# Kernel optimization log

Hardware: AMD Instinct MI355X
Metric: run time of the kernel (lower is better)

Reference implementation:

```python
import jax, jax.numpy as jnp
import numpy as np

B, S, H = 2, 1024, 2048
HQ, HKV, D = 16, 4, 128
E, K, CAP = 32, 4, 512
IM, SIM = 512, 1024
EPS = 1e-6
THETA = 1.0e6
T = B * S


def setup_inputs() -> dict:
    key = jax.random.key(0)
    ks = jax.random.split(key, 16)
    r = lambda i, shape, s=0.02: jax.random.normal(ks[i], shape, dtype=jnp.float32) * s
    return {
        "hidden_states": jax.random.normal(ks[0], (T, H), dtype=jnp.float32),
        "positions": jnp.tile(jnp.arange(S, dtype=jnp.int32), B),
        "ln1_w": jnp.ones((H,), jnp.float32),
        "ln2_w": jnp.ones((H,), jnp.float32),
        "wq": r(1, (H, HQ * D)),
        "wk": r(2, (H, HKV * D)),
        "wv": r(3, (H, HKV * D)),
        "wo": r(4, (HQ * D, H)),
        "qn_w": jnp.ones((D,), jnp.float32),
        "kn_w": jnp.ones((D,), jnp.float32),
        "gate_w": r(5, (H, E), 0.05),
        "expert_bias": r(6, (E,), 0.1),
        "w_gate_e": r(7, (E, H, IM)),
        "w_up_e": r(8, (E, H, IM)),
        "w_down_e": r(9, (E, IM, H)),
        "ws_gate": r(10, (H, SIM)),
        "ws_up": r(11, (H, SIM)),
        "ws_down": r(12, (SIM, H)),
    }


def _rms(x, w):
    return x * jax.lax.rsqrt(jnp.mean(x * x, axis=-1, keepdims=True) + EPS) * w


def _forward(hidden_states, positions, ln1_w, ln2_w, wq, wk, wv, wo, qn_w, kn_w,
             gate_w, expert_bias, w_gate_e, w_up_e, w_down_e, ws_gate, ws_up, ws_down):
    # --- attention block ---
    resid = hidden_states
    h = _rms(hidden_states, ln1_w)
    q = (h @ wq).reshape(T, HQ, D)
    k = (h @ wk).reshape(T, HKV, D)
    v = (h @ wv).reshape(T, HKV, D)
    q = _rms(q, qn_w)  # per-head qk-norm
    k = _rms(k, kn_w)
    # neox-style RoPE over full head_dim
    inv = 1.0 / (THETA ** (jnp.arange(0, D, 2, dtype=jnp.float32) / D))
    fr = positions.astype(jnp.float32)[:, None] * inv  # [T, D/2]
    cos, sin = jnp.cos(fr)[:, None, :], jnp.sin(fr)[:, None, :]
    def rope(x):
        x1, x2 = jnp.split(x, 2, axis=-1)
        return jnp.concatenate([x1 * cos - x2 * sin, x2 * cos + x1 * sin], axis=-1)
    q, k = rope(q), rope(k)
    qb = q.reshape(B, S, HQ, D)
    kb = jnp.repeat(k.reshape(B, S, HKV, D), HQ // HKV, axis=2)  # GQA expand
    vb = jnp.repeat(v.reshape(B, S, HKV, D), HQ // HKV, axis=2)
    sc = jnp.einsum('bqhd,bkhd->bhqk', qb, kb) * (D ** -0.5)
    causal = jnp.tril(jnp.ones((S, S), dtype=bool))
    sc = jnp.where(causal, sc, jnp.float32(-1e30))
    p = jax.nn.softmax(sc, axis=-1)
    ao = jnp.einsum('bhqk,bkhd->bqhd', p, vb).reshape(T, HQ * D)
    h = ao @ wo + resid
    resid = h
    h = _rms(h, ln2_w)
    # --- shared experts (dense MLP) ---
    shared = (jax.nn.silu(h @ ws_gate) * (h @ ws_up)) @ ws_down
    # --- sigmoid router with correction bias (bias only for selection) ---
    scores = jax.nn.sigmoid(h @ gate_w)          # [T, E]
    _, idx = jax.lax.top_k(scores + expert_bias, K)
    w = jnp.take_along_axis(scores, idx, axis=-1)
    w = w / jnp.sum(w, axis=-1, keepdims=True)   # renormalize top-k probs
    # --- capacity-based dispatch / grouped GEMM / combine ---
    flat_e = idx.reshape(-1)                     # [T*K]
    flat_t = jnp.repeat(jnp.arange(T), K)
    flat_w = w.reshape(-1)
    order = jnp.argsort(flat_e)                  # stable sort by expert
    se, st, sw = flat_e[order], flat_t[order], flat_w[order]
    counts = jnp.bincount(flat_e, length=E)
    starts = jnp.concatenate([jnp.zeros((1,), counts.dtype), jnp.cumsum(counts)[:-1]])
    pos = jnp.arange(T * K) - starts[se]         # slot within expert
    valid = pos < CAP                            # capacity guard (never trips in practice)
    posc = jnp.minimum(pos, CAP - 1)
    xbuf = jnp.zeros((E, CAP, H), h.dtype).at[se, posc].add(
        jnp.where(valid[:, None], h[st], 0.0))   # [E, CAP, H]
    inter = jax.nn.silu(jnp.einsum('ech,ehi->eci', xbuf, w_gate_e)) \
            * jnp.einsum('ech,ehi->eci', xbuf, w_up_e)
    obuf = jnp.einsum('eci,eih->ech', inter, w_down_e)
    y = obuf[se, posc] * jnp.where(valid, sw, 0.0)[:, None]
    moe = jnp.zeros((T, H), h.dtype).at[st].add(y)
    return resid + moe + shared


def reference(hidden_states, positions, ln1_w, ln2_w, wq, wk, wv, wo, qn_w, kn_w,
              gate_w, expert_bias, w_gate_e, w_up_e, w_down_e, ws_gate, ws_up, ws_down):
    return _forward(hidden_states, positions, ln1_w, ln2_w, wq, wk, wv, wo, qn_w, kn_w,
                    gate_w, expert_bias, w_gate_e, w_up_e, w_down_e, ws_gate, ws_up, ws_down)
```

## Files before the change

kernel.cpp:

```cpp
#include <hip/hip_runtime.h>
#include <stdint.h>

typedef unsigned short u16;
typedef unsigned short bf16u;
typedef unsigned int u32;
typedef _Float16 f16;
typedef __attribute__((ext_vector_type(8))) short bf16x8;
typedef __attribute__((ext_vector_type(8))) _Float16 f16x8;
typedef __attribute__((ext_vector_type(4))) float f32x4;

#define T_N 2048
#define H_N 2048
#define S_N 1024
#define B_N 2
#define HQ_N 16
#define HKV_N 4
#define D_N 128
#define E_N 32
#define K_TOP 4
#define CAP_N 512
#define IM_N 512
#define SIM_N 1024
#define QD_N 2048
#define KD_N 512
#define QKV_N 3072
#define NFLAT (T_N*K_TOP)
#define RGRP 128
#define NGRP (NFLAT/RGRP)

#define SC_H1   1024.0f
#define SC_W    512.0f
#define SC_QK   2048.0f
#define SC_P    4096.0f
#define SC_V    2048.0f
#define OSC_QKV (1.0f/524288.0f)
#define OSC_OPJ (1.0f/1048576.0f)

__device__ __forceinline__ float bf2f(bf16u x){ return __uint_as_float(((u32)x)<<16); }
__device__ __forceinline__ bf16u f2bf(float f){
  u32 u = __float_as_uint(f);
  u32 r = (u + 0x7FFFu + ((u>>16)&1u)) >> 16;
  return (bf16u)r;
}
__device__ __forceinline__ u32 pkbf(float a, float b){
  u32 ua = __float_as_uint(a), ub = __float_as_uint(b);
  u32 ra = (ua + 0x7FFFu + ((ua>>16)&1u)) >> 16;
  u32 rb = (ub + 0x7FFFu + ((ub>>16)&1u)) & 0xFFFF0000u;
  return ra | rb;
}
__device__ __forceinline__ void split2h(float x, u16& h, u16& l){
  f16 hh = (f16)x;
  f16 ll = (f16)(x - (float)hh);
  h = __builtin_bit_cast(u16, hh);
  l = __builtin_bit_cast(u16, ll);
}
__device__ __forceinline__ f32x4 mfma16b(bf16x8 a, bf16x8 b, f32x4 c){
  return __builtin_amdgcn_mfma_f32_16x16x32_bf16(a,b,c,0,0,0);
}
__device__ __forceinline__ f32x4 mfma16h(f16x8 a, f16x8 b, f32x4 c){
  return __builtin_amdgcn_mfma_f32_16x16x32_f16(a,b,c,0,0,0);
}
__device__ __forceinline__ void gl_lds16(const void* g, void* l){
  __builtin_amdgcn_global_load_lds((const __attribute__((address_space(1))) u32*)g,
                                   (__attribute__((address_space(3))) u32*)l, 16, 0, 0);
}

__global__ __launch_bounds__(256) void transpose_f32(const float* __restrict__ in,
                                                     float* __restrict__ out, int R, int C){
  __shared__ float tile[32][33];
  int rb = blockIdx.x*32, cb = blockIdx.y*32;
  int tx = threadIdx.x, ty = threadIdx.y;
  #pragma unroll
  for (int kk=0;kk<4;kk++)
    tile[ty+kk*8][tx] = in[(size_t)(rb+ty+kk*8)*C + cb + tx];
  __syncthreads();
  #pragma unroll
  for (int kk=0;kk<4;kk++)
    out[(size_t)(cb+ty+kk*8)*R + rb + tx] = tile[tx][ty+kk*8];
}

__global__ __launch_bounds__(256) void transpose_cvt_g(const float* __restrict__ in,
                                                       bf16u* __restrict__ out, int R, int C){
  __shared__ float tile[64*64];
  size_t zo = (size_t)blockIdx.z * R * C;
  int rb = blockIdx.x*64, cb = blockIdx.y*64;
  int tid = threadIdx.x, wave = tid>>6, lane = tid&63;
  #pragma unroll
  for (int p=0;p<4;p++){
    int r = p*16 + wave*4 + (lane>>4);
    const float* src = in + zo + (size_t)(rb + r)*C + cb + (lane&15)*4;
    gl_lds16(src, &tile[(p*16 + wave*4)*64]);
  }
  __syncthreads();
  int c = tid>>2, rq = (tid&3)*16;
  u16 tmp[16];
  #pragma unroll
  for (int j=0;j<16;j++) tmp[j] = f2bf(tile[(rq+j)*64 + c]);
  uint4 w0, w1;
  w0.x=(u32)tmp[0]|((u32)tmp[1]<<16);  w0.y=(u32)tmp[2]|((u32)tmp[3]<<16);
  w0.z=(u32)tmp[4]|((u32)tmp[5]<<16);  w0.w=(u32)tmp[6]|((u32)tmp[7]<<16);
  w1.x=(u32)tmp[8]|((u32)tmp[9]<<16);  w1.y=(u32)tmp[10]|((u32)tmp[11]<<16);
  w1.z=(u32)tmp[12]|((u32)tmp[13]<<16); w1.w=(u32)tmp[14]|((u32)tmp[15]<<16);
  bf16u* dst = out + zo + (size_t)(cb+c)*R + rb + rq;
  *(uint4*)dst = w0;
  *(uint4*)(dst+8) = w1;
}

__global__ __launch_bounds__(256) void transpose_cvt_split16(const float* __restrict__ in,
                                                             u16* __restrict__ oh,
                                                             u16* __restrict__ ol,
                                                             int R, int C, float scale){
  __shared__ u16 th[32][33];
  __shared__ u16 tl[32][33];
  int rb = blockIdx.x*32, cb = blockIdx.y*32;
  int tx = threadIdx.x, ty = threadIdx.y;
  #pragma unroll
  for (int kk=0;kk<4;kk++){
    float x = in[(size_t)(rb+ty+kk*8)*C + cb + tx] * scale;
    u16 hh, ll; split2h(x, hh, ll);
    th[ty+kk*8][tx] = hh; tl[ty+kk*8][tx] = ll;
  }
  __syncthreads();
  #pragma unroll
  for (int kk=0;kk<4;kk++){
    size_t idx = (size_t)(cb+ty+kk*8)*R + rb + tx;
    oh[idx] = th[tx][ty+kk*8];
    ol[idx] = tl[tx][ty+kk*8];
  }
}

__global__ __launch_bounds__(256) void rmsnorm_bf16(const float* __restrict__ x,
                                                    const float* __restrict__ w,
                                                    bf16u* __restrict__ y){
  int row = blockIdx.x; int t = threadIdx.x;
  const float4* x4 = (const float4*)(x + (size_t)row*H_N);
  float4 a = x4[2*t], b = x4[2*t+1];
  float ss = a.x*a.x+a.y*a.y+a.z*a.z+a.w*a.w + b.x*b.x+b.y*b.y+b.z*b.z+b.w*b.w;
  #pragma unroll
  for (int m=32;m>=1;m>>=1) ss += __shfl_xor(ss,m,64);
  __shared__ float red[4];
  if ((t&63)==0) red[t>>6]=ss;
  __syncthreads();
  float scale = rsqrtf((red[0]+red[1]+red[2]+red[3])*(1.0f/H_N) + 1e-6f);
  const float4* w4 = (const float4*)w;
  float4 wa = w4[2*t], wb = w4[2*t+1];
  uint4 pk;
  pk.x = pkbf(a.x*scale*wa.x, a.y*scale*wa.y);
  pk.y = pkbf(a.z*scale*wa.z, a.w*scale*wa.w);
  pk.z = pkbf(b.x*scale*wb.x, b.y*scale*wb.y);
  pk.w = pkbf(b.z*scale*wb.z, b.w*scale*wb.w);
  ((uint4*)(y + (size_t)row*H_N))[t] = pk;
}

__global__ __launch_bounds__(256) void rmsnorm_f16split(const float* __restrict__ x,
                                                        const float* __restrict__ w,
                                                        u16* __restrict__ yh,
                                                        u16* __restrict__ yl){
  int row = blockIdx.x; int t = threadIdx.x;
  const float4* x4 = (const float4*)(x + (size_t)row*H_N);
  float4 a = x4[2*t], b = x4[2*t+1];
  float ss = a.x*a.x+a.y*a.y+a.z*a.z+a.w*a.w + b.x*b.x+b.y*b.y+b.z*b.z+b.w*b.w;
  #pragma unroll
  for (int m=32;m>=1;m>>=1) ss += __shfl_xor(ss,m,64);
  __shared__ float red[4];
  if ((t&63)==0) red[t>>6]=ss;
  __syncthreads();
  float scale = rsqrtf((red[0]+red[1]+red[2]+red[3])*(1.0f/H_N) + 1e-6f) * SC_H1;
  const float4* w4 = (const float4*)w;
  float4 wa = w4[2*t], wb = w4[2*t+1];
  float o[8] = {a.x*scale*wa.x, a.y*scale*wa.y, a.z*scale*wa.z, a.w*scale*wa.w,
                b.x*scale*wb.x, b.y*scale*wb.y, b.z*scale*wb.z, b.w*scale*wb.w};
  u16 hh[8], ll[8];
  #pragma unroll
  for (int j=0;j<8;j++) split2h(o[j], hh[j], ll[j]);
  uint4 pk, pl;
  pk.x = (u32)hh[0]|((u32)hh[1]<<16); pk.y = (u32)hh[2]|((u32)hh[3]<<16);
  pk.z = (u32)hh[4]|((u32)hh[5]<<16); pk.w = (u32)hh[6]|((u32)hh[7]<<16);
  pl.x = (u32)ll[0]|((u32)ll[1]<<16); pl.y = (u32)ll[2]|((u32)ll[3]<<16);
  pl.z = (u32)ll[4]|((u32)ll[5]<<16); pl.w = (u32)ll[6]|((u32)ll[7]<<16);
  ((uint4*)(yh + (size_t)row*H_N))[t] = pk;
  ((uint4*)(yl + (size_t)row*H_N))[t] = pl;
}

__global__ void qknorm_rope_split(const float* __restrict__ qkv,
                                  const float* __restrict__ qw, const float* __restrict__ kw,
                                  const int* __restrict__ positions,
                                  u16* __restrict__ qho, u16* __restrict__ qlo,
                                  u16* __restrict__ kho, u16* __restrict__ klo){
  int t = blockIdx.x; int hy = blockIdx.y; int l = threadIdx.x;
  const float* p; const float* w; u16 *oh, *ol; size_t obase;
  if (hy < HQ_N){
    p = qkv + (size_t)t*QKV_N + hy*D_N; w = qw;
    oh = qho; ol = qlo; obase = (size_t)t*QD_N + hy*D_N;
  } else {
    p = qkv + (size_t)t*QKV_N + QD_N + (hy-HQ_N)*D_N; w = kw;
    oh = kho; ol = klo; obase = (size_t)t*KD_N + (hy-HQ_N)*D_N;
  }
  float x0 = p[l], x1 = p[l+64];
  float ss = x0*x0 + x1*x1;
  #pragma unroll
  for (int m=32;m>=1;m>>=1) ss += __shfl_xor(ss,m,64);
  float scale = rsqrtf(ss*(1.0f/D_N)+1e-6f);
  x0 *= scale*w[l]; x1 *= scale*w[l+64];
  double freq = exp2(-(double)l * (19.931568569324174/64.0));
  double fr = (double)positions[t] * freq;
  double sd, cd; sincos(fr, &sd, &cd);
  float r0 = (float)((double)x0*cd - (double)x1*sd) * SC_QK;
  float r1 = (float)((double)x1*cd + (double)x0*sd) * SC_QK;
  u16 hh, ll;
  split2h(r0, hh, ll); oh[obase+l] = hh; ol[obase+l] = ll;
  split2h(r1, hh, ll); oh[obase+l+64] = hh; ol[obase+l+64] = ll;
}

__global__ __launch_bounds__(256) void transpose_v_split(const float* __restrict__ in,
                                                         u16* __restrict__ oh,
                                                         u16* __restrict__ ol){
  __shared__ u16 th[32][33];
  __shared__ u16 tl[32][33];
  int z = blockIdx.z; int b = z >> 2, kvh = z & 3;
  const float* ip = in + (size_t)b*S_N*QKV_N + QD_N + KD_N + kvh*D_N;
  size_t ob = (size_t)z*D_N*S_N;
  int sb = blockIdx.x*32, db = blockIdx.y*32;
  int tx=threadIdx.x, ty=threadIdx.y;
  #pragma unroll
  for (int kk=0;kk<4;kk++){
    float x = ip[(size_t)(sb+ty+kk*8)*QKV_N + db+tx] * SC_V;
    u16 hh, ll; split2h(x, hh, ll);
    th[ty+kk*8][tx] = hh; tl[ty+kk*8][tx] = ll;
  }
  __syncthreads();
  #pragma unroll
  for (int kk=0;kk<4;kk++){
    size_t idx = ob + (size_t)(db+ty+kk*8)*S_N + sb+tx;
    oh[idx] = th[tx][ty+kk*8];
    ol[idx] = tl[tx][ty+kk*8];
  }
}

template<int MODE, bool SPLIT>
__global__ __launch_bounds__(256) void gemm_bt(
    const u16* __restrict__ A, const u16* __restrict__ Al,
    const u16* __restrict__ B0g, const u16* __restrict__ B0lg,
    const u16* __restrict__ B1g,
    void* __restrict__ Cout, const float* __restrict__ resid, float oscale,
    int N, int Kd,
    const int* __restrict__ startsA, const int* __restrict__ countsA,
    const int* __restrict__ perm)
{
  constexpr bool DUAL = (MODE==2 || MODE==3);
  constexpr bool MOE  = (MODE==3 || MODE==4);
  __shared__ u16 As[2][128*32];
  __shared__ u16 Bs0[2][128*32];
  __shared__ u16 Asl[SPLIT?2:1][SPLIT?128*32:8];
  __shared__ u16 Bs0l[SPLIT?2:1][SPLIT?128*32:8];
  __shared__ u16 Bs1[DUAL?2:1][DUAL?128*32:8];

  int tid = threadIdx.x;
  int wave = tid>>6, lane = tid&63, l15 = lane&15, lg = lane>>4;
  int nBase = blockIdx.y*128;

  int mBase, rows, slotBase=0;
  const u16* Bp0 = B0g; const u16* Bp1 = B1g;
  if constexpr (MOE){
    int e = blockIdx.z;
    int cnt = countsA[e]; cnt = cnt < CAP_N ? cnt : CAP_N;
    mBase = blockIdx.x*128;
    rows = cnt - mBase;
    if (rows <= 0) return;
    if (rows > 128) rows = 128;
    slotBase = startsA[e] + mBase;
    Bp0 = B0g + (size_t)e*N*Kd;
    if constexpr (DUAL) Bp1 = B1g + (size_t)e*N*Kd;
  } else { mBase = blockIdx.x*128; rows = 128; }

  size_t aOff[2], bOff[2];
  #pragma unroll
  for (int i=0;i<2;i++){
    int le = (i*256 + tid)*8;
    int r = le >> 5;
    int c = le & 31;
    int rr = (r < rows) ? r : 0;
    size_t arow;
    if constexpr (MODE==3) arow = (size_t)perm[slotBase + rr];
    else if constexpr (MODE==4) arow = (size_t)(slotBase + rr);
    else arow = (size_t)(mBase + r);
    aOff[i] = arow*Kd + c;
    bOff[i] = (size_t)(nBase + r)*Kd + c;
  }

  auto STAGE = [&](int buf, int kt){
    size_t ko = (size_t)kt*32;
    #pragma unroll
    for (int i=0;i<2;i++){
      int lo = i*2048 + wave*512;
      gl_lds16(A + aOff[i] + ko, &As[buf][lo]);
      gl_lds16(Bp0 + bOff[i] + ko, &Bs0[buf][lo]);
      if constexpr (SPLIT){
        gl_lds16(Al + aOff[i] + ko, &Asl[buf][lo]);
        gl_lds16(B0lg + bOff[i] + ko, &Bs0l[buf][lo]);
      }
      if constexpr (DUAL){
        gl_lds16(Bp1 + bOff[i] + ko, &Bs1[buf][lo]);
      }
    }
  };

  f32x4 zero4 = {0.f,0.f,0.f,0.f};
  f32x4 acc0[4][4];
  f32x4 acc1[DUAL?4:1][DUAL?4:1];
  #pragma unroll
  for (int mi=0;mi<4;mi++)
    #pragma unroll
    for (int ni=0;ni<4;ni++){
      acc0[mi][ni] = zero4;
      if constexpr (DUAL) acc1[mi][ni] = zero4;
    }

  int wm = wave>>1, wn = wave&1;
  int nK = Kd >> 5;
  STAGE(0, 0);
  __syncthreads();
  for (int kt=0; kt<nK; kt++){
    int cur = kt&1;
    if (kt+1 < nK) STAGE(cur^1, kt+1);
    if constexpr (SPLIT){
      f16x8 af[4], afl[4];
      #pragma unroll
      for (int mi=0;mi<4;mi++){
        af[mi]  = *(const f16x8*)&As [cur][(wm*64 + mi*16 + l15)*32 + lg*8];
        afl[mi] = *(const f16x8*)&Asl[cur][(wm*64 + mi*16 + l15)*32 + lg*8];
      }
      #pragma unroll
      for (int ni=0;ni<4;ni++){
        f16x8 b0  = *(const f16x8*)&Bs0 [cur][(wn*64 + ni*16 + l15)*32 + lg*8];
        f16x8 b0l = *(const f16x8*)&Bs0l[cur][(wn*64 + ni*16 + l15)*32 + lg*8];
        #pragma unroll
        for (int mi=0;mi<4;mi++){
          acc0[mi][ni] = mfma16h(af[mi], b0, acc0[mi][ni]);
          acc0[mi][ni] = mfma16h(af[mi], b0l, acc0[mi][ni]);
          acc0[mi][ni] = mfma16h(afl[mi], b0, acc0[mi][ni]);
        }
      }
    } else {
      bf16x8 af[4];
      #pragma unroll
      for (int mi=0;mi<4;mi++)
        af[mi] = *(const bf16x8*)&As[cur][(wm*64 + mi*16 + l15)*32 + lg*8];
      #pragma unroll
      for (int ni=0;ni<4;ni++){
        bf16x8 b0 = *(const bf16x8*)&Bs0[cur][(wn*64 + ni*16 + l15)*32 + lg*8];
        #pragma unroll
        for (int mi=0;mi<4;mi++) acc0[mi][ni] = mfma16b(af[mi], b0, acc0[mi][ni]);
        if constexpr (DUAL){
          bf16x8 b1 = *(const bf16x8*)&Bs1[cur][(wn*64 + ni*16 + l15)*32 + lg*8];
          #pragma unroll
          for (int mi=0;mi<4;mi++) acc1[mi][ni] = mfma16b(af[mi], b1, acc1[mi][ni]);
        }
      }
    }
    __syncthreads();
  }

  #pragma unroll
  for (int mi=0;mi<4;mi++){
    #pragma unroll
    for (int ni=0;ni<4;ni++){
      #pragma unroll
      for (int i=0;i<4;i++){
        int rloc = wm*64 + mi*16 + 4*lg + i;
        int col  = nBase + wn*64 + ni*16 + l15;
        float v = acc0[mi][ni][i];
        if constexpr (MODE==1){
          size_t idx = (size_t)(mBase + rloc)*N + col;
          ((float*)Cout)[idx] = v*oscale + (resid ? resid[idx] : 0.0f);
        } else if constexpr (MODE==2){
          float u = acc1[mi][ni][i];
          float sv = v/(1.0f+__expf(-v))*u;
          ((bf16u*)Cout)[(size_t)(mBase + rloc)*N + col] = f2bf(sv);
        } else if constexpr (MODE==3){
          if (rloc < rows){
            float u = acc1[mi][ni][i];
            float sv = v/(1.0f+__expf(-v))*u;
            ((bf16u*)Cout)[(size_t)(slotBase + rloc)*N + col] = f2bf(sv);
          }
        } else {
          if (rloc < rows)
            ((bf16u*)Cout)[(size_t)(slotBase + rloc)*N + col] = f2bf(v);
        }
      }
    }
  }
}

__global__ __launch_bounds__(256) void attn_kernel(
    const u16* __restrict__ qh, const u16* __restrict__ ql,
    const u16* __restrict__ kh, const u16* __restrict__ kl,
    const u16* __restrict__ vth, const u16* __restrict__ vtl,
    u16* __restrict__ aoh, u16* __restrict__ aol)
{
  int qb = blockIdx.x*64;
  int bh = blockIdx.y;
  int b = bh >> 4, h = bh & 15, kvh = h >> 2;
  int tid = threadIdx.x, wave = tid>>6, lane = tid&63, l15 = lane&15, lg = lane>>4;

  __shared__ u16 Ksh[64*136];
  __shared__ u16 Ksl[64*136];
  __shared__ u16 Vsh[128*72];
  __shared__ u16 Vsl[128*72];
  __shared__ u16 Psh[4][16*72];
  __shared__ u16 Psl[4][16*72];

  size_t qrow = (size_t)(b*S_N + qb + wave*16 + l15)*QD_N + h*D_N;
  f16x8 qfh[4], qfl[4];
  #pragma unroll
  for (int ds=0; ds<4; ds++){
    qfh[ds] = *(const f16x8*)(qh + qrow + ds*32 + lg*8);
    qfl[ds] = *(const f16x8*)(ql + qrow + ds*32 + lg*8);
  }

  f32x4 zero4 = {0.f,0.f,0.f,0.f};
  f32x4 accO[8];
  #pragma unroll
  for (int dc=0; dc<8; dc++) accO[dc] = zero4;
  float mrun[4], lrun[4];
  #pragma unroll
  for (int i=0;i<4;i++){ mrun[i] = -3.0e38f; lrun[i] = 0.0f; }

  const float SC_S = 0.08838834764831845f * (1.0f/(SC_QK*SC_QK));
  int nkt = (qb >> 6) + 1;
  for (int kt=0; kt<nkt; kt++){
    #pragma unroll
    for (int pp=0; pp<4; pp++){
      int r = pp*16 + (tid>>4), c = (tid&15)*8;
      size_t go = (size_t)(b*S_N + kt*64 + r)*KD_N + kvh*D_N + c;
      *(f16x8*)&Ksh[r*136 + c] = *(const f16x8*)(kh + go);
      *(f16x8*)&Ksl[r*136 + c] = *(const f16x8*)(kl + go);
    }
    #pragma unroll
    for (int pp=0; pp<4; pp++){
      int r = pp*32 + (tid>>3), c = (tid&7)*8;
      size_t go = ((size_t)(b*HKV_N + kvh)*D_N + r)*S_N + kt*64 + c;
      *(f16x8*)&Vsh[r*72 + c] = *(const f16x8*)(vth + go);
      *(f16x8*)&Vsl[r*72 + c] = *(const f16x8*)(vtl + go);
    }
    __syncthreads();

    f32x4 sacc[4];
    #pragma unroll
    for (int kc=0;kc<4;kc++){
      sacc[kc] = zero4;
      #pragma unroll
      for (int ds=0; ds<4; ds++){
        f16x8 kfh = *(const f16x8*)&Ksh[(kc*16 + l15)*136 + ds*32 + lg*8];
        f16x8 kfl = *(const f16x8*)&Ksl[(kc*16 + l15)*136 + ds*32 + lg*8];
        sacc[kc] = mfma16h(qfh[ds], kfh, sacc[kc]);
        sacc[kc] = mfma16h(qfh[ds], kfl, sacc[kc]);
        sacc[kc] = mfma16h(qfl[ds], kfh, sacc[kc]);
      }
    }

    float pv[4][4];
    bool last = (kt == nkt-1);
    #pragma unroll
    for (int kc=0;kc<4;kc++)
      #pragma unroll
      for (int i=0;i<4;i++){
        float sv = sacc[kc][i] * SC_S;
        if (last){
          int kg = kt*64 + kc*16 + l15;
          int qg = qb + wave*16 + 4*lg + i;
          if (kg > qg) sv = -3.0e38f;
        }
        pv[kc][i] = sv;
      }

    #pragma unroll
    for (int i=0;i<4;i++){
      float mx = fmaxf(fmaxf(pv[0][i],pv[1][i]),fmaxf(pv[2][i],pv[3][i]));
      #pragma unroll
      for (int mm=1; mm<16; mm<<=1) mx = fmaxf(mx, __shfl_xor(mx, mm, 64));
      float mnew = fmaxf(mrun[i], mx);
      float corr = exp2f((mrun[i]-mnew)*1.44269504f);
      float ps = 0.f;
      #pragma unroll
      for (int kc=0;kc<4;kc++){
        float p = exp2f((pv[kc][i]-mnew)*1.44269504f);
        pv[kc][i] = p; ps += p;
      }
      #pragma unroll
      for (int mm=1; mm<16; mm<<=1) ps += __shfl_xor(ps, mm, 64);
      lrun[i] = lrun[i]*corr + ps;
      mrun[i] = mnew;
      #pragma unroll
      for (int dc=0;dc<8;dc++) accO[dc][i] *= corr;
    }

    #pragma unroll
    for (int kc=0;kc<4;kc++)
      #pragma unroll
      for (int i=0;i<4;i++){
        u16 hh, ll; split2h(pv[kc][i]*SC_P, hh, ll);
        Psh[wave][(4*lg+i)*72 + kc*16 + l15] = hh;
        Psl[wave][(4*lg+i)*72 + kc*16 + l15] = ll;
      }
    asm volatile("s_waitcnt lgkmcnt(0)" ::: "memory");
    __builtin_amdgcn_sched_barrier(0);

    #pragma unroll
    for (int ks=0; ks<2; ks++){
      f16x8 pfh = *(const f16x8*)&Psh[wave][l15*72 + ks*32 + lg*8];
      f16x8 pfl = *(const f16x8*)&Psl[wave][l15*72 + ks*32 + lg*8];
      #pragma unroll
      for (int dc=0; dc<8; dc++){
        f16x8 vfh = *(const f16x8*)&Vsh[(dc*16 + l15)*72 + ks*32 + lg*8];
        f16x8 vfl = *(const f16x8*)&Vsl[(dc*16 + l15)*72 + ks*32 + lg*8];
        accO[dc] = mfma16h(pfh, vfh, accO[dc]);
        accO[dc] = mfma16h(pfh, vfl, accO[dc]);
        accO[dc] = mfma16h(pfl, vfh, accO[dc]);
      }
    }
    __syncthreads();
  }

  #pragma unroll
  for (int i=0;i<4;i++){
    float inv = 1.0f / (4096.0f * lrun[i]);
    size_t orow = (size_t)(b*S_N + qb + wave*16 + 4*lg + i)*QD_N + h*D_N;
    #pragma unroll
    for (int dc=0; dc<8; dc++){
      u16 hh, ll; split2h(accO[dc][i]*inv, hh, ll);
      aoh[orow + dc*16 + l15] = hh;
      aol[orow + dc*16 + l15] = ll;
    }
  }
}

__global__ __launch_bounds__(256) void router_kernel(
    const float* __restrict__ resid2, const float* __restrict__ ln2w,
    const float* __restrict__ gwT, const float* __restrict__ ebias,
    int* __restrict__ tkIdx, float* __restrict__ tkW, int* __restrict__ counts)
{
  int t = blockIdx.x, tid = threadIdx.x;
  __shared__ float xs[H_N];
  __shared__ float red[4];
  __shared__ float sc[E_N];
  const float4* x4 = (const float4*)(resid2 + (size_t)t*H_N);
  float4 a = x4[2*tid], b = x4[2*tid+1];
  float ss = a.x*a.x+a.y*a.y+a.z*a.z+a.w*a.w + b.x*b.x+b.y*b.y+b.z*b.z+b.w*b.w;
  #pragma unroll
  for (int m=32;m>=1;m>>=1) ss += __shfl_xor(ss,m,64);
  if ((tid&63)==0) red[tid>>6]=ss;
  __syncthreads();
  float scale = rsqrtf((red[0]+red[1]+red[2]+red[3])*(1.0f/H_N) + 1e-6f);
  const float4* w4 = (const float4*)ln2w;
  float4 wa = w4[2*tid], wb = w4[2*tid+1];
  xs[tid*8+0]=a.x*scale*wa.x; xs[tid*8+1]=a.y*scale*wa.y;
  xs[tid*8+2]=a.z*scale*wa.z; xs[tid*8+3]=a.w*scale*wa.w;
  xs[tid*8+4]=b.x*scale*wb.x; xs[tid*8+5]=b.y*scale*wb.y;
  xs[tid*8+6]=b.z*scale*wb.z; xs[tid*8+7]=b.w*scale*wb.w;
  __syncthreads();
  int wave = tid>>6, lane = tid&63;
  const float4* xv4 = (const float4*)xs;
  #pragma unroll
  for (int ei=0; ei<8; ei++){
    int e = wave*8 + ei;
    const float4* g4 = (const float4*)(gwT + (size_t)e*H_N);
    float acc = 0.f;
    #pragma unroll
    for (int it=0; it<8; it++){
      int idx = it*64 + lane;
      float4 g = g4[idx], xv = xv4[idx];
      acc += g.x*xv.x + g.y*xv.y + g.z*xv.z + g.w*xv.w;
    }
    #pragma unroll
    for (int m=32;m>=1;m>>=1) acc += __shfl_xor(acc,m,64);
    if (lane==0) sc[e] = 1.0f/(1.0f+__expf(-acc));
  }
  __syncthreads();
  if (tid==0){
    float sb[E_N];
    #pragma unroll
    for (int e2=0;e2<E_N;e2++) sb[e2] = sc[e2]+ebias[e2];
    int ch[4]; float wv[4]; float wsum=0.f;
    for (int j=0;j<4;j++){
      int best=0; float bv=-3.0e38f;
      for (int e2=0;e2<E_N;e2++) if (sb[e2] > bv){ bv=sb[e2]; best=e2; }
      ch[j]=best; wv[j]=sc[best]; wsum+=sc[best]; sb[best]=-3.0e38f;
    }
    float invs = 1.0f/wsum;
    for (int j=0;j<4;j++){
      tkIdx[t*4+j]=ch[j]; tkW[t*4+j]=wv[j]*invs;
      atomicAdd(&counts[ch[j]], 1);
    }
  }
}

__global__ void moe_count_kernel(const int* __restrict__ tki, int* __restrict__ G){
  __shared__ int cnt[E_N];
  int g = blockIdx.x, t = threadIdx.x;
  if (t < E_N) cnt[t] = 0;
  __syncthreads();
  atomicAdd(&cnt[tki[g*RGRP + t]], 1);
  __syncthreads();
  if (t < E_N) G[g*E_N + t] = cnt[t];
}

__global__ void moe_scan_kernel(const int* __restrict__ G, int* __restrict__ base,
                                int* __restrict__ starts){
  __shared__ int tot[E_N];
  int e = threadIdx.x;
  if (e < E_N){
    int run = 0;
    for (int g=0; g<NGRP; g++){ base[g*E_N+e] = run; run += G[g*E_N+e]; }
    tot[e] = run < CAP_N ? run : CAP_N;
  }
  __syncthreads();
  if (e==0){
    int run=0;
    for (int x=0; x<E_N; x++){ starts[x]=run; run+=tot[x]; }
  }
}

__global__ void moe_assign_kernel(const int* __restrict__ tki,
                                  const int* __restrict__ base, const int* __restrict__ starts,
                                  int* __restrict__ ptok, int* __restrict__ tok2slot){
  __shared__ int eL[RGRP];
  int g = blockIdx.x, t = threadIdx.x;
  int f = g*RGRP + t;
  int e = tki[f];
  eL[t] = e;
  __syncthreads();
  int r = 0;
  for (int j=0; j<RGRP; j++) r += ((j < t) && (eL[j]==e)) ? 1 : 0;
  int pos = base[g*E_N + e] + r;
  if (pos < CAP_N){
    int slot = starts[e] + pos;
    ptok[slot] = f >> 2;
    tok2slot[f] = slot;
  } else {
    tok2slot[f] = -1;
  }
}

__global__ __launch_bounds__(256) void moe_combine(const int* __restrict__ tok2slot,
                                                   const float* __restrict__ tkw,
                                                   const bf16u* __restrict__ obuf,
                                                   float* __restrict__ outp){
  int t = blockIdx.x;
  int c0 = threadIdx.x*8;
  float acc[8];
  float4* o4 = (float4*)(outp + (size_t)t*H_N + c0);
  float4 v0 = o4[0], v1 = o4[1];
  acc[0]=v0.x; acc[1]=v0.y; acc[2]=v0.z; acc[3]=v0.w;
  acc[4]=v1.x; acc[5]=v1.y; acc[6]=v1.z; acc[7]=v1.w;
  #pragma unroll
  for (int j=0;j<4;j++){
    int slot = tok2slot[t*4+j];
    if (slot >= 0){
      float w = tkw[t*4+j];
      bf16x8 ob = *(const bf16x8*)(obuf + (size_t)slot*H_N + c0);
      #pragma unroll
      for (int q=0;q<8;q++) acc[q] += w * bf2f((bf16u)ob[q]);
    }
  }
  v0.x=acc[0]; v0.y=acc[1]; v0.z=acc[2]; v0.w=acc[3];
  v1.x=acc[4]; v1.y=acc[5]; v1.z=acc[6]; v1.w=acc[7];
  o4[0]=v0; o4[1]=v1;
}

extern "C" void kernel_launch(void* const* d_in, const int* in_sizes, int n_in,
                              void* d_out, int out_size, void* d_ws, size_t ws_size,
                              hipStream_t stream) {
  (void)in_sizes; (void)n_in; (void)out_size; (void)ws_size;
  const float* hidden    = (const float*)d_in[0];
  const int*   positions = (const int*)d_in[1];
  const float* ln1w = (const float*)d_in[2];
  const float* ln2w = (const float*)d_in[3];
  const float* wq   = (const float*)d_in[4];
  const float* wk   = (const float*)d_in[5];
  const float* wv   = (const float*)d_in[6];
  const float* wo   = (const float*)d_in[7];
  const float* qnw  = (const float*)d_in[8];
  const float* knw  = (const float*)d_in[9];
  const float* gatew= (const float*)d_in[10];
  const float* ebias= (const float*)d_in[11];
  const float* wge  = (const float*)d_in[12];
  const float* wue  = (const float*)d_in[13];
  const float* wde  = (const float*)d_in[14];
  const float* wsg  = (const float*)d_in[15];
  const float* wsu  = (const float*)d_in[16];
  const float* wsd  = (const float*)d_in[17];
  float* outp = (float*)d_out;

  char* wsb = (char*)d_ws;
  size_t off = 0;
  auto take = [&](size_t bytes)->char*{
    char* p = wsb + off; off += (bytes + 255) & ~(size_t)255; return p;
  };
  u16* qkvTh = (u16*)take(3072ull*2048*2);
  u16* qkvTl = (u16*)take(3072ull*2048*2);
  u16* woTh = (u16*)take(2048ull*2048*2);
  u16* woTl = (u16*)take(2048ull*2048*2);
  u16* wsgT = (u16*)take(1024ull*2048*2);
  u16* wsuT = (u16*)take(1024ull*2048*2);
  u16* wsdT = (u16*)take(2048ull*1024*2);
  u16* wgeT = (u16*)take(32ull*512*2048*2);
  u16* wueT = (u16*)take(32ull*512*2048*2);
  u16* wdeT = (u16*)take(32ull*2048*512*2);
  float* gwT = (float*)take(32ull*2048*4);
  u16* h1h  = (u16*)take((size_t)T_N*H_N*2);
  u16* h1l  = (u16*)take((size_t)T_N*H_N*2);
  float* qkv32 = (float*)take((size_t)T_N*QKV_N*4);
  u16* qHh  = (u16*)take((size_t)T_N*QD_N*2);
  u16* qHl  = (u16*)take((size_t)T_N*QD_N*2);
  u16* kHh  = (u16*)take((size_t)T_N*KD_N*2);
  u16* kHl  = (u16*)take((size_t)T_N*KD_N*2);
  u16* vtHh = (u16*)take((size_t)T_N*KD_N*2);
  u16* vtHl = (u16*)take((size_t)T_N*KD_N*2);
  u16* aoh  = (u16*)take((size_t)T_N*QD_N*2);
  u16* aol  = (u16*)take((size_t)T_N*QD_N*2);
  float* resid2=(float*)take((size_t)T_N*H_N*4);
  u16* h2   = (u16*)take((size_t)T_N*H_N*2);
  u16* interS=(u16*)take((size_t)T_N*SIM_N*2);
  u16* minter=(u16*)take((size_t)NFLAT*IM_N*2);
  bf16u* obuf = (bf16u*)take((size_t)NFLAT*H_N*2);
  int*   tki  = (int*)take((size_t)NFLAT*4);
  float* tkw  = (float*)take((size_t)NFLAT*4);
  int*   counts=(int*)take(E_N*4);
  int*   Gcnt = (int*)take((size_t)NGRP*E_N*4);
  int*   Gbase= (int*)take((size_t)NGRP*E_N*4);
  int*   starts=(int*)take(E_N*4);
  int*   ptok = (int*)take((size_t)NFLAT*4);
  int*   tok2slot = (int*)take((size_t)NFLAT*4);

  hipMemsetAsync(counts, 0, 256, stream);

  dim3 tb(32,8);
  transpose_cvt_split16<<<dim3(64,64,1), tb, 0, stream>>>(wq, qkvTh, qkvTl, 2048, 2048, SC_W);
  transpose_cvt_split16<<<dim3(64,16,1), tb, 0, stream>>>(wk, qkvTh + 2048ull*2048, qkvTl + 2048ull*2048, 2048, 512, SC_W);
  transpose_cvt_split16<<<dim3(64,16,1), tb, 0, stream>>>(wv, qkvTh + 2560ull*2048, qkvTl + 2560ull*2048, 2048, 512, SC_W);
  transpose_cvt_split16<<<dim3(64,64,1), tb, 0, stream>>>(wo, woTh, woTl, 2048, 2048, SC_W);
  transpose_cvt_g<<<dim3(32,16,1), 256, 0, stream>>>(wsg, wsgT, 2048, 1024);
  transpose_cvt_g<<<dim3(32,16,1), 256, 0, stream>>>(wsu, wsuT, 2048, 1024);
  transpose_cvt_g<<<dim3(16,32,1), 256, 0, stream>>>(wsd, wsdT, 1024, 2048);
  transpose_cvt_g<<<dim3(32,8,32), 256, 0, stream>>>(wge, wgeT, 2048, 512);
  transpose_cvt_g<<<dim3(32,8,32), 256, 0, stream>>>(wue, wueT, 2048, 512);
  transpose_cvt_g<<<dim3(8,32,32), 256, 0, stream>>>(wde, wdeT, 512, 2048);
  transpose_f32<<<dim3(64,1,1), tb, 0, stream>>>(gatew, gwT, 2048, 32);

  rmsnorm_f16split<<<T_N, 256, 0, stream>>>(hidden, ln1w, h1h, h1l);
  gemm_bt<1,true><<<dim3(16,24), 256, 0, stream>>>(h1h, h1l, qkvTh, qkvTl, nullptr, qkv32, nullptr, OSC_QKV, QKV_N, H_N, nullptr,nullptr,nullptr);
  qknorm_rope_split<<<dim3(T_N,20), 64, 0, stream>>>(qkv32, qnw, knw, positions, qHh, qHl, kHh, kHl);
  transpose_v_split<<<dim3(32,4,8), tb, 0, stream>>>(qkv32, vtHh, vtHl);
  attn_kernel<<<dim3(16,32), 256, 0, stream>>>(qHh, qHl, kHh, kHl, vtHh, vtHl, aoh, aol);
  gemm_bt<1,true><<<dim3(16,16), 256, 0, stream>>>(aoh, aol, woTh, woTl, nullptr, resid2, hidden, OSC_OPJ, H_N, QD_N, nullptr,nullptr,nullptr);
  rmsnorm_bf16<<<T_N, 256, 0, stream>>>(resid2, ln2w, (bf16u*)h2);
  gemm_bt<2,false><<<dim3(16,8), 256, 0, stream>>>(h2, nullptr, wsgT, nullptr, wsuT, interS, nullptr, 1.0f, SIM_N, H_N, nullptr,nullptr,nullptr);
  gemm_bt<1,false><<<dim3(16,16), 256, 0, stream>>>(interS, nullptr, wsdT, nullptr, nullptr, outp, resid2, 1.0f, H_N, SIM_N, nullptr,nullptr,nullptr);
  router_kernel<<<T_N, 256, 0, stream>>>(resid2, ln2w, gwT, ebias, tki, tkw, counts);
  moe_count_kernel<<<NGRP, RGRP, 0, stream>>>(tki, Gcnt);
  moe_scan_kernel<<<1, 64, 0, stream>>>(Gcnt, Gbase, starts);
  moe_assign_kernel<<<NGRP, RGRP, 0, stream>>>(tki, Gbase, starts, ptok, tok2slot);
  gemm_bt<3,false><<<dim3(4,4,32), 256, 0, stream>>>(h2, nullptr, wgeT, nullptr, wueT, minter, nullptr, 1.0f, IM_N, H_N, starts, counts, ptok);
  gemm_bt<4,false><<<dim3(4,16,32), 256, 0, stream>>>(minter, nullptr, wdeT, nullptr, nullptr, obuf, nullptr, 1.0f, H_N, IM_N, starts, counts, nullptr);
  moe_combine<<<T_N, 256, 0, stream>>>(tok2slot, tkw, obuf, outp);
}
```

Baseline: 943.9 us.

## Split MoE expert GEMMs into dedicated kernels with 64-row M tiles

Moves the MoE gate/up and down GEMMs out of the generic templated gemm_bt into two specialised kernels that use 64-row M tiles instead of 128. Each expert holds about 256 tokens on average, so the smaller tiles cut wasted MFMA work on partially filled tiles and launch more blocks for better CU occupancy. The generic GEMM loses its MoE branches, which simplifies its address setup. The cost is that each block reads the expert weight tile twice as often across M, adding weight traffic.

After: 1.024 ms. 8.5% more time.

```diff
diff --git a/kernel.cpp b/kernel.cpp
--- a/kernel.cpp
+++ b/kernel.cpp
@@ -243,12 +243,9 @@
     const u16* __restrict__ B0g, const u16* __restrict__ B0lg,
     const u16* __restrict__ B1g,
     void* __restrict__ Cout, const float* __restrict__ resid, float oscale,
-    int N, int Kd,
-    const int* __restrict__ startsA, const int* __restrict__ countsA,
-    const int* __restrict__ perm)
+    int N, int Kd)
 {
-  constexpr bool DUAL = (MODE==2 || MODE==3);
-  constexpr bool MOE  = (MODE==3 || MODE==4);
+  constexpr bool DUAL = (MODE==2);
   __shared__ u16 As[2][128*32];
   __shared__ u16 Bs0[2][128*32];
   __shared__ u16 Asl[SPLIT?2:1][SPLIT?128*32:8];
@@ -258,20 +255,7 @@
   int tid = threadIdx.x;
   int wave = tid>>6, lane = tid&63, l15 = lane&15, lg = lane>>4;
   int nBase = blockIdx.y*128;
-
-  int mBase, rows, slotBase=0;
-  const u16* Bp0 = B0g; const u16* Bp1 = B1g;
-  if constexpr (MOE){
-    int e = blockIdx.z;
-    int cnt = countsA[e]; cnt = cnt < CAP_N ? cnt : CAP_N;
-    mBase = blockIdx.x*128;
-    rows = cnt - mBase;
-    if (rows <= 0) return;
-    if (rows > 128) rows = 128;
-    slotBase = startsA[e] + mBase;
-    Bp0 = B0g + (size_t)e*N*Kd;
-    if constexpr (DUAL) Bp1 = B1g + (size_t)e*N*Kd;
-  } else { mBase = blockIdx.x*128; rows = 128; }
+  int mBase = blockIdx.x*128;
 
   size_t aOff[2], bOff[2];
   #pragma unroll
@@ -279,12 +263,7 @@
     int le = (i*256 + tid)*8;
     int r = le >> 5;
     int c = le & 31;
-    int rr = (r < rows) ? r : 0;
-    size_t arow;
-    if constexpr (MODE==3) arow = (size_t)perm[slotBase + rr];
-    else if constexpr (MODE==4) arow = (size_t)(slotBase + rr);
-    else arow = (size_t)(mBase + r);
-    aOff[i] = arow*Kd + c;
+    aOff[i] = (size_t)(mBase + r)*Kd + c;
     bOff[i] = (size_t)(nBase + r)*Kd + c;
   }
 
@@ -294,13 +273,13 @@
     for (int i=0;i<2;i++){
       int lo = i*2048 + wave*512;
       gl_lds16(A + aOff[i] + ko, &As[buf][lo]);
-      gl_lds16(Bp0 + bOff[i] + ko, &Bs0[buf][lo]);
+      gl_lds16(B0g + bOff[i] + ko, &Bs0[buf][lo]);
       if constexpr (SPLIT){
         gl_lds16(Al + aOff[i] + ko, &Asl[buf][lo]);
         gl_lds16(B0lg + bOff[i] + ko, &Bs0l[buf][lo]);
       }
       if constexpr (DUAL){
-        gl_lds16(Bp1 + bOff[i] + ko, &Bs1[buf][lo]);
+        gl_lds16(B1g + bOff[i] + ko, &Bs1[buf][lo]);
       }
     }
   };
@@ -373,20 +352,187 @@
         if constexpr (MODE==1){
           size_t idx = (size_t)(mBase + rloc)*N + col;
           ((float*)Cout)[idx] = v*oscale + (resid ? resid[idx] : 0.0f);
-        } else if constexpr (MODE==2){
+        } else {
           float u = acc1[mi][ni][i];
           float sv = v/(1.0f+__expf(-v))*u;
           ((bf16u*)Cout)[(size_t)(mBase + rloc)*N + col] = f2bf(sv);
-        } else if constexpr (MODE==3){
-          if (rloc < rows){
-            float u = acc1[mi][ni][i];
-            float sv = v/(1.0f+__expf(-v))*u;
-            ((bf16u*)Cout)[(size_t)(slotBase + rloc)*N + col] = f2bf(sv);
-          }
-        } else {
-          if (rloc < rows)
-            ((bf16u*)Cout)[(size_t)(slotBase + rloc)*N + col] = f2bf(v);
         }
+      }
+    }
+  }
+}
+
+__global__ __launch_bounds__(256) void moe_gu64(
+    const u16* __restrict__ A,
+    const u16* __restrict__ B0g,
+    const u16* __restrict__ B1g,
+    bf16u* __restrict__ Out,
+    const int* __restrict__ starts, const int* __restrict__ counts,
+    const int* __restrict__ perm)
+{
+  __shared__ u16 As[2][64*32];
+  __shared__ u16 Bs0[2][128*32];
+  __shared__ u16 Bs1[2][128*32];
+
+  int e = blockIdx.z;
+  int cnt = counts[e]; cnt = cnt < CAP_N ? cnt : CAP_N;
+  int mBase = blockIdx.x*64;
+  int rows = cnt - mBase;
+  if (rows <= 0) return;
+  if (rows > 64) rows = 64;
+  int slotBase = starts[e] + mBase;
+  int nBase = blockIdx.y*128;
+  const u16* Bp0 = B0g + (size_t)e*IM_N*H_N;
+  const u16* Bp1 = B1g + (size_t)e*IM_N*H_N;
+
+  int tid = threadIdx.x, wave = tid>>6, lane = tid&63, l15 = lane&15, lg = lane>>4;
+  int ar = tid>>2, ac = (tid&3)*8;
+  int arr = (ar < rows) ? ar : 0;
+  size_t aOff = (size_t)perm[slotBase + arr]*H_N + ac;
+  size_t bOff[2];
+  #pragma unroll
+  for (int i=0;i<2;i++){
+    int le = (i*256 + tid)*8;
+    bOff[i] = (size_t)(nBase + (le>>5))*H_N + (le&31);
+  }
+
+  auto STAGE = [&](int buf, int kt){
+    size_t ko = (size_t)kt*32;
+    gl_lds16(A + aOff + ko, &As[buf][tid*8]);
+    #pragma unroll
+    for (int i=0;i<2;i++){
+      int lo = i*2048 + wave*512;
+      gl_lds16(Bp0 + bOff[i] + ko, &Bs0[buf][lo]);
+      gl_lds16(Bp1 + bOff[i] + ko, &Bs1[buf][lo]);
+    }
+  };
+
+  f32x4 zero4 = {0.f,0.f,0.f,0.f};
+  f32x4 acc0[2][4], acc1[2][4];
+  #pragma unroll
+  for (int mi=0;mi<2;mi++)
+    #pragma unroll
+    for (int ni=0;ni<4;ni++){ acc0[mi][ni]=zero4; acc1[mi][ni]=zero4; }
+
+  int wm = wave>>1, wn = wave&1;
+  STAGE(0, 0);
+  __syncthreads();
+  int nK = H_N >> 5;
+  for (int kt=0; kt<nK; kt++){
+    int cur = kt&1;
+    if (kt+1 < nK) STAGE(cur^1, kt+1);
+    bf16x8 af[2];
+    #pragma unroll
+    for (int mi=0;mi<2;mi++)
+      af[mi] = *(const bf16x8*)&As[cur][(wm*32 + mi*16 + l15)*32 + lg*8];
+    #pragma unroll
+    for (int ni=0;ni<4;ni++){
+      bf16x8 b0 = *(const bf16x8*)&Bs0[cur][(wn*64 + ni*16 + l15)*32 + lg*8];
+      bf16x8 b1 = *(const bf16x8*)&Bs1[cur][(wn*64 + ni*16 + l15)*32 + lg*8];
+      #pragma unroll
+      for (int mi=0;mi<2;mi++){
+        acc0[mi][ni] = mfma16b(af[mi], b0, acc0[mi][ni]);
+        acc1[mi][ni] = mfma16b(af[mi], b1, acc1[mi][ni]);
+      }
+    }
+    __syncthreads();
+  }
+
+  #pragma unroll
+  for (int mi=0;mi<2;mi++){
+    #pragma unroll
+    for (int ni=0;ni<4;ni++){
+      #pragma unroll
+      for (int i=0;i<4;i++){
+        int rloc = wm*32 + mi*16 + 4*lg + i;
+        if (rloc < rows){
+          float v = acc0[mi][ni][i];
+          float u = acc1[mi][ni][i];
+          float sv = v/(1.0f+__expf(-v))*u;
+          Out[(size_t)(slotBase + rloc)*IM_N + nBase + wn*64 + ni*16 + l15] = f2bf(sv);
+        }
+      }
+    }
+  }
+}
+
+__global__ __launch_bounds__(256) void moe_down64(
+    const u16* __restrict__ A,
+    const u16* __restrict__ B0g,
+    bf16u* __restrict__ Out,
+    const int* __restrict__ starts, const int* __restrict__ counts)
+{
+  __shared__ u16 As[2][64*32];
+  __shared__ u16 Bs0[2][128*32];
+
+  int e = blockIdx.z;
+  int cnt = counts[e]; cnt = cnt < CAP_N ? cnt : CAP_N;
+  int mBase = blockIdx.x*64;
+  int rows = cnt - mBase;
+  if (rows <= 0) return;
+  if (rows > 64) rows = 64;
+  int slotBase = starts[e] + mBase;
+  int nBase = blockIdx.y*128;
+  const u16* Bp0 = B0g + (size_t)e*H_N*IM_N;
+
+  int tid = threadIdx.x, wave = tid>>6, lane = tid&63, l15 = lane&15, lg = lane>>4;
+  int ar = tid>>2, ac = (tid&3)*8;
+  int arr = (ar < rows) ? ar : 0;
+  size_t aOff = (size_t)(slotBase + arr)*IM_N + ac;
+  size_t bOff[2];
+  #pragma unroll
+  for (int i=0;i<2;i++){
+    int le = (i*256 + tid)*8;
+    bOff[i] = (size_t)(nBase + (le>>5))*IM_N + (le&31);
+  }
+
+  auto STAGE = [&](int buf, int kt){
+    size_t ko = (size_t)kt*32;
+    gl_lds16(A + aOff + ko, &As[buf][tid*8]);
+    #pragma unroll
+    for (int i=0;i<2;i++){
+      int lo = i*2048 + wave*512;
+      gl_lds16(Bp0 + bOff[i] + ko, &Bs0[buf][lo]);
+    }
+  };
+
+  f32x4 zero4 = {0.f,0.f,0.f,0.f};
+  f32x4 acc0[2][4];
+  #pragma unroll
+  for (int mi=0;mi<2;mi++)
+    #pragma unroll
+    for (int ni=0;ni<4;ni++) acc0[mi][ni]=zero4;
+
+  int wm = wave>>1, wn = wave&1;
+  STAGE(0, 0);
+  __syncthreads();
+  int nK = IM_N >> 5;
+  for (int kt=0; kt<nK; kt++){
+    int cur = kt&1;
+    if (kt+1 < nK) STAGE(cur^1, kt+1);
+    bf16x8 af[2];
+    #pragma unroll
+    for (int mi=0;mi<2;mi++)
+      af[mi] = *(const bf16x8*)&As[cur][(wm*32 + mi*16 + l15)*32 + lg*8];
+    #pragma unroll
+    for (int ni=0;ni<4;ni++){
+      bf16x8 b0 = *(const bf16x8*)&Bs0[cur][(wn*64 + ni*16 + l15)*32 + lg*8];
+      #pragma unroll
+      for (int mi=0;mi<2;mi++)
+        acc0[mi][ni] = mfma16b(af[mi], b0, acc0[mi][ni]);
+    }
+    __syncthreads();
+  }
+
+  #pragma unroll
+  for (int mi=0;mi<2;mi++){
+    #pragma unroll
+    for (int ni=0;ni<4;ni++){
+      #pragma unroll
+      for (int i=0;i<4;i++){
+        int rloc = wm*32 + mi*16 + 4*lg + i;
+        if (rloc < rows)
+          Out[(size_t)(slotBase + rloc)*H_N + nBase + wn*64 + ni*16 + l15] = f2bf(acc0[mi][ni][i]);
       }
     }
   }
@@ -749,19 +895,19 @@
   transpose_f32<<<dim3(64,1,1), tb, 0, stream>>>(gatew, gwT, 2048, 32);
 
   rmsnorm_f16split<<<T_N, 256, 0, stream>>>(hidden, ln1w, h1h, h1l);
-  gemm_bt<1,true><<<dim3(16,24), 256, 0, stream>>>(h1h, h1l, qkvTh, qkvTl, nullptr, qkv32, nullptr, OSC_QKV, QKV_N, H_N, nullptr,nullptr,nullptr);
+  gemm_bt<1,true><<<dim3(16,24), 256, 0, stream>>>(h1h, h1l, qkvTh, qkvTl, nullptr, qkv32, nullptr, OSC_QKV, QKV_N, H_N);
   qknorm_rope_split<<<dim3(T_N,20), 64, 0, stream>>>(qkv32, qnw, knw, positions, qHh, qHl, kHh, kHl);
   transpose_v_split<<<dim3(32,4,8), tb, 0, stream>>>(qkv32, vtHh, vtHl);
   attn_kernel<<<dim3(16,32), 256, 0, stream>>>(qHh, qHl, kHh, kHl, vtHh, vtHl, aoh, aol);
-  gemm_bt<1,true><<<dim3(16,16), 256, 0, stream>>>(aoh, aol, woTh, woTl, nullptr, resid2, hidden, OSC_OPJ, H_N, QD_N, nullptr,nullptr,nullptr);
+  gemm_bt<1,true><<<dim3(16,16), 256, 0, stream>>>(aoh, aol, woTh, woTl, nullptr, resid2, hidden, OSC_OPJ, H_N, QD_N);
   rmsnorm_bf16<<<T_N, 256, 0, stream>>>(resid2, ln2w, (bf16u*)h2);
-  gemm_bt<2,false><<<dim3(16,8), 256, 0, stream>>>(h2, nullptr, wsgT, nullptr, wsuT, interS, nullptr, 1.0f, SIM_N, H_N, nullptr,nullptr,nullptr);
-  gemm_bt<1,false><<<dim3(16,16), 256, 0, stream>>>(interS, nullptr, wsdT, nullptr, nullptr, outp, resid2, 1.0f, H_N, SIM_N, nullptr,nullptr,nullptr);
+  gemm_bt<2,false><<<dim3(16,8), 256, 0, stream>>>(h2, nullptr, wsgT, nullptr, wsuT, interS, nullptr, 1.0f, SIM_N, H_N);
+  gemm_bt<1,false><<<dim3(16,16), 256, 0, stream>>>(interS, nullptr, wsdT, nullptr, nullptr, outp, resid2, 1.0f, H_N, SIM_N);
   router_kernel<<<T_N, 256, 0, stream>>>(resid2, ln2w, gwT, ebias, tki, tkw, counts);
   moe_count_kernel<<<NGRP, RGRP, 0, stream>>>(tki, Gcnt);
   moe_scan_kernel<<<1, 64, 0, stream>>>(Gcnt, Gbase, starts);
   moe_assign_kernel<<<NGRP, RGRP, 0, stream>>>(tki, Gbase, starts, ptok, tok2slot);
-  gemm_bt<3,false><<<dim3(4,4,32), 256, 0, stream>>>(h2, nullptr, wgeT, nullptr, wueT, minter, nullptr, 1.0f, IM_N, H_N, starts, counts, ptok);
-  gemm_bt<4,false><<<dim3(4,16,32), 256, 0, stream>>>(minter, nullptr, wdeT, nullptr, nullptr, obuf, nullptr, 1.0f, H_N, IM_N, starts, counts, nullptr);
+  moe_gu64<<<dim3(8,4,32), 256, 0, stream>>>(h2, wgeT, wueT, minter, starts, counts, ptok);
+  moe_down64<<<dim3(8,16,32), 256, 0, stream>>>(minter, wdeT, obuf, starts, counts);
   moe_combine<<<T_N, 256, 0, stream>>>(tok2slot, tkw, obuf, outp);
 }
```
